# Kernel tuning notes

Measured on AMD Instinct MI355X. Metric: run time of the kernel, lower is better.

## Reference

```python
import jax, jax.numpy as jnp
import numpy as np

N_NODES = 50000
N_EDGES = 100000
IN_FEATS = 32
EDGE_FEATS = 32
HIDDEN = 32
OUT = 3


def setup_inputs() -> dict:
    key = jax.random.key(0)
    ks = jax.random.split(key, 16)
    s = 0.05
    return {
        "node_feats": jax.random.normal(ks[0], (N_NODES, IN_FEATS), jnp.float32),
        "edge_feats": jax.random.normal(ks[1], (N_EDGES, EDGE_FEATS), jnp.float32),
        "src": jax.random.randint(ks[2], (N_EDGES,), 0, N_NODES, jnp.int32),
        "dst": jax.random.randint(ks[3], (N_EDGES,), 0, N_NODES, jnp.int32),
        "edge_indices": jnp.arange(N_EDGES, dtype=jnp.int32),
        # edge_network: Linear(edge_feats, hidden*in) -> ReLU -> Linear(hidden*in, hidden*in)
        "W1": jax.random.normal(ks[4], (EDGE_FEATS, HIDDEN * IN_FEATS), jnp.float32) * s,
        "b1": jax.random.normal(ks[5], (HIDDEN * IN_FEATS,), jnp.float32) * s,
        "W2": jax.random.normal(ks[6], (HIDDEN * IN_FEATS, HIDDEN * IN_FEATS), jnp.float32) * s,
        "b2": jax.random.normal(ks[7], (HIDDEN * IN_FEATS,), jnp.float32) * s,
        # NNConv bias
        "conv_bias": jax.random.normal(ks[8], (HIDDEN,), jnp.float32) * s,
        # edge classifier: Linear(2*hidden+edge_feats, hidden) -> ReLU -> Linear(hidden, out)
        "Wc1": jax.random.normal(ks[9], (2 * HIDDEN + EDGE_FEATS, HIDDEN), jnp.float32) * s,
        "bc1": jax.random.normal(ks[10], (HIDDEN,), jnp.float32) * s,
        "Wc2": jax.random.normal(ks[11], (HIDDEN, OUT), jnp.float32) * s,
        "bc2": jax.random.normal(ks[12], (OUT,), jnp.float32) * s,
    }


def reference(node_feats, edge_feats, src, dst, edge_indices,
              W1, b1, W2, b2, conv_bias, Wc1, bc1, Wc2, bc2):
    N = node_feats.shape[0]
    E = edge_feats.shape[0]
    in_f = node_feats.shape[1]
    hid = conv_bias.shape[0]

    # edge-conditioned weights: MLP(efeat) -> [E, in, hidden]
    w = jax.nn.relu(edge_feats @ W1 + b1) @ W2 + b2
    w = w.reshape(E, in_f, hid)

    # per-edge matmul of gathered src features, then mean-aggregate into dst (DGL NNConv, aggregator='mean')
    msg = jnp.einsum("ei,eio->eo", node_feats[src], w)  # [E, hidden]
    agg = jax.ops.segment_sum(msg, dst, num_segments=N)  # [N, hidden]
    deg = jax.ops.segment_sum(jnp.ones((E,), msg.dtype), dst, num_segments=N)
    agg = agg / jnp.maximum(deg, 1.0)[:, None]
    h = jax.nn.relu(agg + conv_bias)  # [N, hidden]

    # gather-concat-MLP edge classifier
    s = src[edge_indices]
    d = dst[edge_indices]
    edge_in = jnp.concatenate([h[s], h[d], edge_feats[edge_indices]], axis=1)
    logits = jax.nn.relu(edge_in @ Wc1 + bc1) @ Wc2 + bc2
    return logits
```

## Files before the change

kernel.cpp:

```cpp
#include <hip/hip_runtime.h>
#include <hip/hip_bf16.h>
#include <stdint.h>

#define NNODES 50000
#define NEDGES 100000

typedef __attribute__((ext_vector_type(8))) short short8;
typedef __attribute__((ext_vector_type(4))) float f32x4;

__device__ __forceinline__ unsigned short f2bf(float f) {
    union { unsigned int i; float f; } v; v.f = f;
    unsigned int r = v.i + 0x7FFFu + ((v.i >> 16) & 1u);
    return (unsigned short)(r >> 16);
}
__device__ __forceinline__ float bf2f(unsigned short u) {
    union { unsigned int i; float f; } v; v.i = ((unsigned int)u) << 16; return v.f;
}
__device__ __forceinline__ void gload16(const void* g, void* lds) {
    __builtin_amdgcn_global_load_lds(
        (const __attribute__((address_space(1))) unsigned int*)g,
        (__attribute__((address_space(3))) unsigned int*)lds, 16, 0, 0);
}

__global__ __launch_bounds__(256) void k_pack(const float* __restrict__ W2,
                                              unsigned short* __restrict__ w2p) {
    const int idx = blockIdx.x * 256 + threadIdx.x;
    const int k = idx >> 10, col = idx & 1023;
    const float v = W2[idx];
    const int nb = col >> 7, n = col & 127;
    const int ks = k >> 5, kg = (k >> 3) & 3, j = k & 7;
    w2p[((((size_t)nb * 32 + ks) * 4 + kg) * 128 + n) * 8 + j] = f2bf(v);
}

__global__ __launch_bounds__(256) void k_packw1(const float* __restrict__ W1,
                                                unsigned short* __restrict__ w1pT) {
    const int idx = blockIdx.x * 256 + threadIdx.x;
    const int i = idx >> 10, col = idx & 1023;
    const float v = W1[idx];
    const int ks = col >> 5, c = col & 31;
    const int kt = c >> 4, lr = c & 15;
    const int lq = i >> 3, ii = i & 7;
    w1pT[((((size_t)ks * 2 + kt) * 4 + lq) * 16 + lr) * 8 + ii] = f2bf(v);
}

__global__ __launch_bounds__(256, 2) void k_gemm(
    const unsigned short* __restrict__ w2p, const unsigned short* __restrict__ w1pT,
    const float* __restrict__ ef, const float* __restrict__ nf,
    const float* __restrict__ b1, const float* __restrict__ b2,
    const int* __restrict__ src, const int* __restrict__ dst,
    float* __restrict__ agg, float* __restrict__ deg)
{
    __shared__ __align__(16) unsigned short sB[2][8192];
    __shared__ __align__(16) unsigned short sH[2][4096];
    __shared__ __align__(16) unsigned short sXb[4096];
    __shared__ int sD[128];

    const int t    = threadIdx.x;
    const int lane = t & 63;
    const int w    = t >> 6;
    const int wm   = w >> 1, wc = w & 1;
    const int lq   = lane >> 4, lr = lane & 15;
    const int e0   = blockIdx.x * 128;
    const int yb   = blockIdx.y;
    const int nblk0 = yb * 2;

    unsigned short* sE = sB[0];

    {
        const int e = t >> 1, fo = (t & 1) * 16;
        const int eg = e0 + e;
        const bool valid = eg < NEDGES;
        const int iq = fo >> 3;
        unsigned short hh[16];
        uint4 pa, pb;

        #pragma unroll
        for (int q = 0; q < 4; ++q) {
            float4 v = valid ? *(const float4*)(ef + (size_t)eg * 32 + fo + q * 4)
                             : float4{0.f, 0.f, 0.f, 0.f};
            hh[q*4+0] = f2bf(v.x); hh[q*4+1] = f2bf(v.y);
            hh[q*4+2] = f2bf(v.z); hh[q*4+3] = f2bf(v.w);
        }
        pa.x = hh[0] | ((unsigned)hh[1] << 16);  pa.y = hh[2]  | ((unsigned)hh[3] << 16);
        pa.z = hh[4] | ((unsigned)hh[5] << 16);  pa.w = hh[6]  | ((unsigned)hh[7] << 16);
        pb.x = hh[8] | ((unsigned)hh[9] << 16);  pb.y = hh[10] | ((unsigned)hh[11] << 16);
        pb.z = hh[12]| ((unsigned)hh[13] << 16); pb.w = hh[14] | ((unsigned)hh[15] << 16);
        *(uint4*)(sE + ((iq    ) * 128 + e) * 8) = pa;
        *(uint4*)(sE + ((iq + 1) * 128 + e) * 8) = pb;

        const int s = valid ? src[eg] : 0;
        #pragma unroll
        for (int q = 0; q < 4; ++q) {
            float4 xv = valid ? *(const float4*)(nf + (size_t)s * 32 + fo + q * 4)
                              : float4{0.f, 0.f, 0.f, 0.f};
            hh[q*4+0] = f2bf(xv.x); hh[q*4+1] = f2bf(xv.y);
            hh[q*4+2] = f2bf(xv.z); hh[q*4+3] = f2bf(xv.w);
        }
        pa.x = hh[0] | ((unsigned)hh[1] << 16);  pa.y = hh[2]  | ((unsigned)hh[3] << 16);
        pa.z = hh[4] | ((unsigned)hh[5] << 16);  pa.w = hh[6]  | ((unsigned)hh[7] << 16);
        pb.x = hh[8] | ((unsigned)hh[9] << 16);  pb.y = hh[10] | ((unsigned)hh[11] << 16);
        pb.z = hh[12]| ((unsigned)hh[13] << 16); pb.w = hh[14] | ((unsigned)hh[15] << 16);
        *(uint4*)(sXb + ((iq    ) * 128 + e) * 8) = pa;
        *(uint4*)(sXb + ((iq + 1) * 128 + e) * 8) = pb;
    }
    if (t < 128) {
        const int eg = e0 + t;
        const int dv = (eg < NEDGES) ? dst[eg] : -1;
        sD[t] = dv;
        if (yb == 0 && dv >= 0) atomicAdd(&deg[dv], 1.0f);
    }
    __syncthreads();

    const short8 bfe0 = *(const short8*)(sE + (lq * 128 + w * 32 + lr) * 8);
    const short8 bfe1 = *(const short8*)(sE + (lq * 128 + w * 32 + 16 + lr) * 8);

    f32x4 pm[8];
    #pragma unroll
    for (int i = 0; i < 8; ++i) pm[i] = f32x4{0.f, 0.f, 0.f, 0.f};
    if (yb == 0 && wc == 0) {
        short8 bb0, bb1;
        #pragma unroll
        for (int j = 0; j < 8; ++j) {
            bb0[j] = (short)f2bf(b2[(lq * 8 + j) * 32 + lr]);
            bb1[j] = (short)f2bf(b2[(lq * 8 + j) * 32 + 16 + lr]);
        }
        #pragma unroll
        for (int mt = 0; mt < 4; ++mt) {
            const short8 xf = *(const short8*)(sXb + (lq * 128 + wm * 64 + mt * 16 + lr) * 8);
            pm[mt * 2]     = __builtin_amdgcn_mfma_f32_16x16x32_bf16(xf, bb0, pm[mt * 2],     0, 0, 0);
            pm[mt * 2 + 1] = __builtin_amdgcn_mfma_f32_16x16x32_bf16(xf, bb1, pm[mt * 2 + 1], 0, 0, 0);
        }
    }
    __syncthreads();

    #define STAGE2(dstb, nblk_, ks_) do {                                          \
        const unsigned short* _g0 = w2p + ((size_t)((nblk_) * 32 + (ks_)) * 4096); \
        const unsigned short* _g1 = _g0 + (size_t)32 * 4096;                       \
        gload16(_g0 + (size_t)t * 8,         (dstb) + w * 512);                    \
        gload16(_g0 + (size_t)(t + 256) * 8, (dstb) + 2048 + w * 512);             \
        gload16(_g1 + (size_t)t * 8,         (dstb) + 4096 + w * 512);             \
        gload16(_g1 + (size_t)(t + 256) * 8, (dstb) + 6144 + w * 512);             \
    } while (0)

    STAGE2(sB[0], nblk0, 0);

    short8 w1c0 = *(const short8*)(w1pT + ((0 * 4 + lq) * 16 + lr) * 8);
    short8 w1c1 = *(const short8*)(w1pT + ((1 * 4 + lq) * 16 + lr) * 8);
    float4 b1c0 = *(const float4*)(b1 + lq * 4);
    float4 b1c1 = *(const float4*)(b1 + 16 + lq * 4);

    f32x4 acc[4][8];
    #pragma unroll
    for (int mt = 0; mt < 4; ++mt)
        #pragma unroll
        for (int nt = 0; nt < 8; ++nt) acc[mt][nt] = f32x4{0.f, 0.f, 0.f, 0.f};

    int buf = 0;
    for (int ks = 0; ks < 32; ++ks) {
        unsigned short* sHp = sH[ks & 1];

        f32x4 h00 = {b1c0.x, b1c0.y, b1c0.z, b1c0.w};
        f32x4 h01 = h00;
        f32x4 h10 = {b1c1.x, b1c1.y, b1c1.z, b1c1.w};
        f32x4 h11 = h10;
        h00 = __builtin_amdgcn_mfma_f32_16x16x32_bf16(w1c0, bfe0, h00, 0, 0, 0);
        h01 = __builtin_amdgcn_mfma_f32_16x16x32_bf16(w1c0, bfe1, h01, 0, 0, 0);
        h10 = __builtin_amdgcn_mfma_f32_16x16x32_bf16(w1c1, bfe0, h10, 0, 0, 0);
        h11 = __builtin_amdgcn_mfma_f32_16x16x32_bf16(w1c1, bfe1, h11, 0, 0, 0);

        #define STORE_H1(hv, kt, et) do {                                           \
            float r0 = fmaxf((hv)[0], 0.f), r1 = fmaxf((hv)[1], 0.f);               \
            float r2 = fmaxf((hv)[2], 0.f), r3 = fmaxf((hv)[3], 0.f);               \
            unsigned p0, p1;                                                         \
            asm("v_cvt_pk_bf16_f32 %0, %1, %2" : "=v"(p0) : "v"(r0), "v"(r1));       \
            asm("v_cvt_pk_bf16_f32 %0, %1, %2" : "=v"(p1) : "v"(r2), "v"(r3));       \
            uint2 pk; pk.x = p0; pk.y = p1;                                          \
            *(uint2*)(sHp + ((((kt) * 2 + (lq >> 1)) * 128 + w * 32 + (et) * 16 + lr)\
                * 8 + (lq & 1) * 4)) = pk;                                           \
        } while (0)
        STORE_H1(h00, 0, 0); STORE_H1(h01, 0, 1);
        STORE_H1(h10, 1, 0); STORE_H1(h11, 1, 1);
        #undef STORE_H1

        __syncthreads();

        if (ks != 31) STAGE2(sB[buf ^ 1], nblk0, ks + 1);
        const int nks2 = (ks == 31) ? 0 : ks + 1;
        short8 w1n0 = *(const short8*)(w1pT + ((((size_t)nks2 * 2 + 0) * 4 + lq) * 16 + lr) * 8);
        short8 w1n1 = *(const short8*)(w1pT + ((((size_t)nks2 * 2 + 1) * 4 + lq) * 16 + lr) * 8);
        float4 b1n0 = *(const float4*)(b1 + nks2 * 32 + lq * 4);
        float4 b1n1 = *(const float4*)(b1 + nks2 * 32 + 16 + lq * 4);

        const short8 af0 = *(const short8*)(sHp + (lq * 128 + wm * 64 +  0 + lr) * 8);
        const short8 af1 = *(const short8*)(sHp + (lq * 128 + wm * 64 + 16 + lr) * 8);
        const short8 af2 = *(const short8*)(sHp + (lq * 128 + wm * 64 + 32 + lr) * 8);
        const short8 af3 = *(const short8*)(sHp + (lq * 128 + wm * 64 + 48 + lr) * 8);
        const unsigned short* pb = sB[buf] + wc * 4096;
        __builtin_amdgcn_s_setprio(1);
        #pragma unroll
        for (int nt = 0; nt < 8; ++nt) {
            const short8 bf = *(const short8*)(pb + (lq * 128 + nt * 16 + lr) * 8);
            acc[0][nt] = __builtin_amdgcn_mfma_f32_16x16x32_bf16(af0, bf, acc[0][nt], 0, 0, 0);
            acc[1][nt] = __builtin_amdgcn_mfma_f32_16x16x32_bf16(af1, bf, acc[1][nt], 0, 0, 0);
            acc[2][nt] = __builtin_amdgcn_mfma_f32_16x16x32_bf16(af2, bf, acc[2][nt], 0, 0, 0);
            acc[3][nt] = __builtin_amdgcn_mfma_f32_16x16x32_bf16(af3, bf, acc[3][nt], 0, 0, 0);
        }
        __builtin_amdgcn_s_setprio(0);
        buf ^= 1;
        w1c0 = w1n0; w1c1 = w1n1; b1c0 = b1n0; b1c1 = b1n1;
    }

    {
        const int nblk = nblk0 + wc;
        #pragma unroll
        for (int ii = 0; ii < 4; ++ii) {
            const int i  = nblk * 4 + ii;
            const int iq = i >> 3, io = i & 7;
            #pragma unroll
            for (int mt = 0; mt < 4; ++mt)
                #pragma unroll
                for (int r = 0; r < 4; ++r) {
                    const int e = wm * 64 + mt * 16 + lq * 4 + r;
                    const float x = bf2f(sXb[iq * 1024 + e * 8 + io]);
                    pm[mt*2+0][r] = fmaf(x, acc[mt][ii*2+0][r], pm[mt*2+0][r]);
                    pm[mt*2+1][r] = fmaf(x, acc[mt][ii*2+1][r], pm[mt*2+1][r]);
                }
        }
    }
    #undef STAGE2

    __syncthreads();
    float* sRed = (float*)sB;
    if (wc == 0) {
        #pragma unroll
        for (int mt = 0; mt < 4; ++mt)
            #pragma unroll
            for (int r = 0; r < 4; ++r) {
                const int e = wm * 64 + mt * 16 + lq * 4 + r;
                sRed[e * 36 + lr]      = pm[mt*2][r];
                sRed[e * 36 + 16 + lr] = pm[mt*2+1][r];
            }
    }
    __syncthreads();
    if (wc == 1) {
        #pragma unroll
        for (int mt = 0; mt < 4; ++mt)
            #pragma unroll
            for (int r = 0; r < 4; ++r) {
                const int e = wm * 64 + mt * 16 + lq * 4 + r;
                sRed[e * 36 + lr]      += pm[mt*2][r];
                sRed[e * 36 + 16 + lr] += pm[mt*2+1][r];
            }
    }
    __syncthreads();

    #pragma unroll
    for (int mt = 0; mt < 2; ++mt)
        #pragma unroll
        for (int r = 0; r < 4; ++r) {
            const int e = w * 32 + mt * 16 + lq * 4 + r;
            const int d = sD[e];
            if (d >= 0) {
                atomicAdd(agg + (size_t)d * 32 + lr,      sRed[e * 36 + lr]);
                atomicAdd(agg + (size_t)d * 32 + 16 + lr, sRed[e * 36 + 16 + lr]);
            }
        }
}

__global__ __launch_bounds__(256) void k_node(
    float* __restrict__ agg, const float* __restrict__ deg,
    const float* __restrict__ cbias)
{
    const int idx = blockIdx.x * 256 + threadIdx.x;
    if (idx >= NNODES * 32) return;
    const int n = idx >> 5, o = idx & 31;
    const float d = fmaxf(deg[n], 1.0f);
    agg[idx] = fmaxf(agg[idx] / d + cbias[o], 0.0f);
}

__global__ __launch_bounds__(256) void k_cls(
    const float* __restrict__ h, const float* __restrict__ ef,
    const int* __restrict__ src, const int* __restrict__ dst,
    const int* __restrict__ eidx,
    const float* __restrict__ Wc1, const float* __restrict__ bc1,
    const float* __restrict__ Wc2, const float* __restrict__ bc2,
    float* __restrict__ out)
{
    __shared__ float s_w1[96 * 32];
    __shared__ float s_w2[96];
    __shared__ float s_b1[32];
    __shared__ float s_in[8][96];

    const int t = threadIdx.x;
    #pragma unroll
    for (int q = 0; q < 3; ++q)
        *(float4*)&s_w1[t * 12 + q * 4] = *(const float4*)&Wc1[t * 12 + q * 4];
    if (t < 96) s_w2[t] = Wc2[t];
    if (t >= 96 && t < 128) s_b1[t - 96] = bc1[t - 96];

    const int ee = t >> 5, l = t & 31;
    const int e  = blockIdx.x * 8 + ee;
    const int ei = eidx[e];
    const int s = src[ei], d = dst[ei];
    s_in[ee][l]      = h[(size_t)s * 32 + l];
    s_in[ee][32 + l] = h[(size_t)d * 32 + l];
    s_in[ee][64 + l] = ef[(size_t)ei * 32 + l];
    __syncthreads();

    float acc = s_b1[l];
    #pragma unroll
    for (int c = 0; c < 96; ++c) acc = fmaf(s_in[ee][c], s_w1[c * 32 + l], acc);
    acc = fmaxf(acc, 0.f);

    float p0 = acc * s_w2[l * 3 + 0];
    float p1 = acc * s_w2[l * 3 + 1];
    float p2 = acc * s_w2[l * 3 + 2];
    #pragma unroll
    for (int m = 1; m <= 16; m <<= 1) {
        p0 += __shfl_xor(p0, m);
        p1 += __shfl_xor(p1, m);
        p2 += __shfl_xor(p2, m);
    }
    if (l == 0) {
        out[(size_t)e * 3 + 0] = p0 + bc2[0];
        out[(size_t)e * 3 + 1] = p1 + bc2[1];
        out[(size_t)e * 3 + 2] = p2 + bc2[2];
    }
}

extern "C" void kernel_launch(void* const* d_in, const int* in_sizes, int n_in,
                              void* d_out, int out_size, void* d_ws, size_t ws_size,
                              hipStream_t stream) {
    const float* nf   = (const float*)d_in[0];
    const float* ef   = (const float*)d_in[1];
    const int*   src  = (const int*)d_in[2];
    const int*   dst  = (const int*)d_in[3];
    const int*   eidx = (const int*)d_in[4];
    const float* W1   = (const float*)d_in[5];
    const float* b1   = (const float*)d_in[6];
    const float* W2   = (const float*)d_in[7];
    const float* b2   = (const float*)d_in[8];
    const float* cb   = (const float*)d_in[9];
    const float* Wc1  = (const float*)d_in[10];
    const float* bc1  = (const float*)d_in[11];
    const float* Wc2  = (const float*)d_in[12];
    const float* bc2  = (const float*)d_in[13];
    float* out = (float*)d_out;

    float* agg = (float*)d_ws;
    float* deg = agg + (size_t)NNODES * 32;
    unsigned short* w2p  = (unsigned short*)(deg + NNODES);
    unsigned short* w1pT = w2p + 1048576;

    hipMemsetAsync(d_ws, 0, ((size_t)NNODES * 32 + NNODES) * 4, stream);
    k_pack<<<4096, 256, 0, stream>>>(W2, w2p);
    k_packw1<<<128, 256, 0, stream>>>(W1, w1pT);

    k_gemm<<<dim3((NEDGES + 127) / 128, 4), 256, 0, stream>>>(
        w2p, w1pT, ef, nf, b1, b2, src, dst, agg, deg);

    k_node<<<(NNODES * 32 + 255) / 256, 256, 0, stream>>>(agg, deg, cb);
    k_cls<<<NEDGES / 8, 256, 0, stream>>>(agg, ef, src, dst, eidx, Wc1, bc1, Wc2, bc2, out);
}
```

Before: 334.9 us.

## Switch edge-network GEMM to 32x32x16 MFMA and software-pipeline hidden-layer production

Replaces the 16x16x32 bf16 MFMA tiles with 32x32x16 tiles for the W1 hidden layer, the W2 GEMM, and the bias term, and repacks W1 to match the new operand layout. The next K-slice of the hidden activations is now produced while the current slice's B fragments are loaded, so each K step needs one barrier instead of two. The aim is fewer MFMA issues and LDS fragment reads per FLOP, plus less barrier stalling. The cost is more live registers (preloaded fragments for both k-chunks), which could hurt occupancy under launch_bounds(256,2).

```diff
diff --git a/kernel.cpp b/kernel.cpp
--- a/kernel.cpp
+++ b/kernel.cpp
@@ -7,6 +7,7 @@
 
 typedef __attribute__((ext_vector_type(8))) short short8;
 typedef __attribute__((ext_vector_type(4))) float f32x4;
+typedef __attribute__((ext_vector_type(16))) float f32x16;
 
 __device__ __forceinline__ unsigned short f2bf(float f) {
     union { unsigned int i; float f; } v; v.f = f;
@@ -35,12 +36,10 @@
 __global__ __launch_bounds__(256) void k_packw1(const float* __restrict__ W1,
                                                 unsigned short* __restrict__ w1pT) {
     const int idx = blockIdx.x * 256 + threadIdx.x;
-    const int i = idx >> 10, col = idx & 1023;
-    const float v = W1[idx];
-    const int ks = col >> 5, c = col & 31;
-    const int kt = c >> 4, lr = c & 15;
-    const int lq = i >> 3, ii = i & 7;
-    w1pT[((((size_t)ks * 2 + kt) * 4 + lq) * 16 + lr) * 8 + ii] = f2bf(v);
+    const int ii = idx & 7, lane = (idx >> 3) & 63, ic = (idx >> 9) & 1, ks = idx >> 10;
+    const int i = ic * 16 + (lane >> 5) * 8 + ii;
+    const int k = ks * 32 + (lane & 31);
+    w1pT[idx] = f2bf(W1[(size_t)i * 1024 + k]);
 }
 
 __global__ __launch_bounds__(256, 2) void k_gemm(
@@ -59,6 +58,7 @@
     const int lane = t & 63;
     const int w    = t >> 6;
     const int wm   = w >> 1, wc = w & 1;
+    const int lo5  = lane & 31, hi = lane >> 5;
     const int lq   = lane >> 4, lr = lane & 15;
     const int e0   = blockIdx.x * 128;
     const int yb   = blockIdx.y;
@@ -111,26 +111,63 @@
     }
     __syncthreads();
 
-    const short8 bfe0 = *(const short8*)(sE + (lq * 128 + w * 32 + lr) * 8);
-    const short8 bfe1 = *(const short8*)(sE + (lq * 128 + w * 32 + 16 + lr) * 8);
-
-    f32x4 pm[8];
-    #pragma unroll
-    for (int i = 0; i < 8; ++i) pm[i] = f32x4{0.f, 0.f, 0.f, 0.f};
+    const short8 bfe0 = *(const short8*)(sE + ((0 + hi) * 128 + w * 32 + lo5) * 8);
+    const short8 bfe1 = *(const short8*)(sE + ((2 + hi) * 128 + w * 32 + lo5) * 8);
+
+    f32x16 pm[2];
+    #pragma unroll
+    for (int mt = 0; mt < 2; ++mt)
+        #pragma unroll
+        for (int r = 0; r < 16; ++r) pm[mt][r] = 0.f;
     if (yb == 0 && wc == 0) {
-        short8 bb0, bb1;
-        #pragma unroll
-        for (int j = 0; j < 8; ++j) {
-            bb0[j] = (short)f2bf(b2[(lq * 8 + j) * 32 + lr]);
-            bb1[j] = (short)f2bf(b2[(lq * 8 + j) * 32 + 16 + lr]);
-        }
-        #pragma unroll
-        for (int mt = 0; mt < 4; ++mt) {
-            const short8 xf = *(const short8*)(sXb + (lq * 128 + wm * 64 + mt * 16 + lr) * 8);
-            pm[mt * 2]     = __builtin_amdgcn_mfma_f32_16x16x32_bf16(xf, bb0, pm[mt * 2],     0, 0, 0);
-            pm[mt * 2 + 1] = __builtin_amdgcn_mfma_f32_16x16x32_bf16(xf, bb1, pm[mt * 2 + 1], 0, 0, 0);
-        }
-    }
+        short8 b2f0, b2f1;
+        #pragma unroll
+        for (int ii = 0; ii < 8; ++ii) {
+            b2f0[ii] = (short)f2bf(b2[(     hi * 8 + ii) * 32 + lo5]);
+            b2f1[ii] = (short)f2bf(b2[(16 + hi * 8 + ii) * 32 + lo5]);
+        }
+        #pragma unroll
+        for (int mt = 0; mt < 2; ++mt) {
+            const short8 xa0 = *(const short8*)(sXb + ((0 + hi) * 128 + wm * 64 + mt * 32 + lo5) * 8);
+            const short8 xa1 = *(const short8*)(sXb + ((2 + hi) * 128 + wm * 64 + mt * 32 + lo5) * 8);
+            pm[mt] = __builtin_amdgcn_mfma_f32_32x32x16_bf16(xa0, b2f0, pm[mt], 0, 0, 0);
+            pm[mt] = __builtin_amdgcn_mfma_f32_32x32x16_bf16(xa1, b2f1, pm[mt], 0, 0, 0);
+        }
+    }
+
+    #define H1_PRODUCE(ks2_, dstp_, wA_, wB_) do {                                   \
+        f32x16 hacc;                                                                  \
+        _Pragma("unroll")                                                             \
+        for (int q = 0; q < 4; ++q) {                                                 \
+            const float4 blo = *(const float4*)(b1 + (ks2_) * 32 + q * 8);            \
+            const float4 bhi = *(const float4*)(b1 + (ks2_) * 32 + q * 8 + 4);        \
+            hacc[q*4+0] = hi ? bhi.x : blo.x;                                         \
+            hacc[q*4+1] = hi ? bhi.y : blo.y;                                         \
+            hacc[q*4+2] = hi ? bhi.z : blo.z;                                         \
+            hacc[q*4+3] = hi ? bhi.w : blo.w;                                         \
+        }                                                                             \
+        hacc = __builtin_amdgcn_mfma_f32_32x32x16_bf16((wA_), bfe0, hacc, 0, 0, 0);   \
+        hacc = __builtin_amdgcn_mfma_f32_32x32x16_bf16((wB_), bfe1, hacc, 0, 0, 0);   \
+        _Pragma("unroll")                                                             \
+        for (int q = 0; q < 4; ++q) {                                                 \
+            float v0 = fmaxf(hacc[q*4+0], 0.f), v1 = fmaxf(hacc[q*4+1], 0.f);         \
+            float v2 = fmaxf(hacc[q*4+2], 0.f), v3 = fmaxf(hacc[q*4+3], 0.f);         \
+            unsigned p0, p1;                                                          \
+            asm("v_cvt_pk_bf16_f32 %0, %1, %2" : "=v"(p0) : "v"(v0), "v"(v1));        \
+            asm("v_cvt_pk_bf16_f32 %0, %1, %2" : "=v"(p1) : "v"(v2), "v"(v3));        \
+            uint2 pk; pk.x = p0; pk.y = p1;                                           \
+            *(uint2*)((dstp_) + q * 1024 + (w * 32 + lo5) * 8 + hi * 4) = pk;         \
+        }                                                                             \
+    } while (0)
+
+    {
+        const short8 wA = *(const short8*)(w1pT + ((size_t)(0 * 2 + 0) * 64 + lane) * 8);
+        const short8 wB = *(const short8*)(w1pT + ((size_t)(0 * 2 + 1) * 64 + lane) * 8);
+        H1_PRODUCE(0, sH[0], wA, wB);
+    }
+    short8 w1cA = *(const short8*)(w1pT + ((size_t)(1 * 2 + 0) * 64 + lane) * 8);
+    short8 w1cB = *(const short8*)(w1pT + ((size_t)(1 * 2 + 1) * 64 + lane) * 8);
+
     __syncthreads();
 
     #define STAGE2(dstb, nblk_, ks_) do {                                          \
@@ -144,112 +181,87 @@
 
     STAGE2(sB[0], nblk0, 0);
 
-    short8 w1c0 = *(const short8*)(w1pT + ((0 * 4 + lq) * 16 + lr) * 8);
-    short8 w1c1 = *(const short8*)(w1pT + ((1 * 4 + lq) * 16 + lr) * 8);
-    float4 b1c0 = *(const float4*)(b1 + lq * 4);
-    float4 b1c1 = *(const float4*)(b1 + 16 + lq * 4);
-
-    f32x4 acc[4][8];
-    #pragma unroll
-    for (int mt = 0; mt < 4; ++mt)
-        #pragma unroll
-        for (int nt = 0; nt < 8; ++nt) acc[mt][nt] = f32x4{0.f, 0.f, 0.f, 0.f};
+    f32x16 acc[2][4];
+    #pragma unroll
+    for (int mt = 0; mt < 2; ++mt)
+        #pragma unroll
+        for (int nt = 0; nt < 4; ++nt)
+            #pragma unroll
+            for (int r = 0; r < 16; ++r) acc[mt][nt][r] = 0.f;
 
     int buf = 0;
     for (int ks = 0; ks < 32; ++ks) {
-        unsigned short* sHp = sH[ks & 1];
-
-        f32x4 h00 = {b1c0.x, b1c0.y, b1c0.z, b1c0.w};
-        f32x4 h01 = h00;
-        f32x4 h10 = {b1c1.x, b1c1.y, b1c1.z, b1c1.w};
-        f32x4 h11 = h10;
-        h00 = __builtin_amdgcn_mfma_f32_16x16x32_bf16(w1c0, bfe0, h00, 0, 0, 0);
-        h01 = __builtin_amdgcn_mfma_f32_16x16x32_bf16(w1c0, bfe1, h01, 0, 0, 0);
-        h10 = __builtin_amdgcn_mfma_f32_16x16x32_bf16(w1c1, bfe0, h10, 0, 0, 0);
-        h11 = __builtin_amdgcn_mfma_f32_16x16x32_bf16(w1c1, bfe1, h11, 0, 0, 0);
-
-        #define STORE_H1(hv, kt, et) do {                                           \
-            float r0 = fmaxf((hv)[0], 0.f), r1 = fmaxf((hv)[1], 0.f);               \
-            float r2 = fmaxf((hv)[2], 0.f), r3 = fmaxf((hv)[3], 0.f);               \
-            unsigned p0, p1;                                                         \
-            asm("v_cvt_pk_bf16_f32 %0, %1, %2" : "=v"(p0) : "v"(r0), "v"(r1));       \
-            asm("v_cvt_pk_bf16_f32 %0, %1, %2" : "=v"(p1) : "v"(r2), "v"(r3));       \
-            uint2 pk; pk.x = p0; pk.y = p1;                                          \
-            *(uint2*)(sHp + ((((kt) * 2 + (lq >> 1)) * 128 + w * 32 + (et) * 16 + lr)\
-                * 8 + (lq & 1) * 4)) = pk;                                           \
-        } while (0)
-        STORE_H1(h00, 0, 0); STORE_H1(h01, 0, 1);
-        STORE_H1(h10, 1, 0); STORE_H1(h11, 1, 1);
-        #undef STORE_H1
-
         __syncthreads();
 
         if (ks != 31) STAGE2(sB[buf ^ 1], nblk0, ks + 1);
-        const int nks2 = (ks == 31) ? 0 : ks + 1;
-        short8 w1n0 = *(const short8*)(w1pT + ((((size_t)nks2 * 2 + 0) * 4 + lq) * 16 + lr) * 8);
-        short8 w1n1 = *(const short8*)(w1pT + ((((size_t)nks2 * 2 + 1) * 4 + lq) * 16 + lr) * 8);
-        float4 b1n0 = *(const float4*)(b1 + nks2 * 32 + lq * 4);
-        float4 b1n1 = *(const float4*)(b1 + nks2 * 32 + 16 + lq * 4);
-
-        const short8 af0 = *(const short8*)(sHp + (lq * 128 + wm * 64 +  0 + lr) * 8);
-        const short8 af1 = *(const short8*)(sHp + (lq * 128 + wm * 64 + 16 + lr) * 8);
-        const short8 af2 = *(const short8*)(sHp + (lq * 128 + wm * 64 + 32 + lr) * 8);
-        const short8 af3 = *(const short8*)(sHp + (lq * 128 + wm * 64 + 48 + lr) * 8);
+
+        const unsigned short* pa = sH[ks & 1];
         const unsigned short* pb = sB[buf] + wc * 4096;
+        short8 af0[2], af1[2], bfr[2][4];
+        #pragma unroll
+        for (int kc = 0; kc < 2; ++kc) {
+            af0[kc] = *(const short8*)(pa + ((kc * 2 + hi) * 128 + wm * 64 +  0 + lo5) * 8);
+            af1[kc] = *(const short8*)(pa + ((kc * 2 + hi) * 128 + wm * 64 + 32 + lo5) * 8);
+            #pragma unroll
+            for (int nt = 0; nt < 4; ++nt)
+                bfr[kc][nt] = *(const short8*)(pb + ((kc * 2 + hi) * 128 + nt * 32 + lo5) * 8);
+        }
+
+        if (ks < 31) {
+            H1_PRODUCE(ks + 1, sH[(ks + 1) & 1], w1cA, w1cB);
+            const int nk2 = (ks < 30) ? ks + 2 : 31;
+            w1cA = *(const short8*)(w1pT + ((size_t)(nk2 * 2 + 0) * 64 + lane) * 8);
+            w1cB = *(const short8*)(w1pT + ((size_t)(nk2 * 2 + 1) * 64 + lane) * 8);
+        }
+
         __builtin_amdgcn_s_setprio(1);
         #pragma unroll
-        for (int nt = 0; nt < 8; ++nt) {
-            const short8 bf = *(const short8*)(pb + (lq * 128 + nt * 16 + lr) * 8);
-            acc[0][nt] = __builtin_amdgcn_mfma_f32_16x16x32_bf16(af0, bf, acc[0][nt], 0, 0, 0);
-            acc[1][nt] = __builtin_amdgcn_mfma_f32_16x16x32_bf16(af1, bf, acc[1][nt], 0, 0, 0);
-            acc[2][nt] = __builtin_amdgcn_mfma_f32_16x16x32_bf16(af2, bf, acc[2][nt], 0, 0, 0);
-            acc[3][nt] = __builtin_amdgcn_mfma_f32_16x16x32_bf16(af3, bf, acc[3][nt], 0, 0, 0);
+        for (int kc = 0; kc < 2; ++kc) {
+            #pragma unroll
+            for (int nt = 0; nt < 4; ++nt) {
+                acc[0][nt] = __builtin_amdgcn_mfma_f32_32x32x16_bf16(af0[kc], bfr[kc][nt], acc[0][nt], 0, 0, 0);
+                acc[1][nt] = __builtin_amdgcn_mfma_f32_32x32x16_bf16(af1[kc], bfr[kc][nt], acc[1][nt], 0, 0, 0);
+            }
         }
         __builtin_amdgcn_s_setprio(0);
         buf ^= 1;
-        w1c0 = w1n0; w1c1 = w1n1; b1c0 = b1n0; b1c1 = b1n1;
-    }
-
-    {
-        const int nblk = nblk0 + wc;
-        #pragma unroll
-        for (int ii = 0; ii < 4; ++ii) {
-            const int i  = nblk * 4 + ii;
-            const int iq = i >> 3, io = i & 7;
-            #pragma unroll
-            for (int mt = 0; mt < 4; ++mt)
-                #pragma unroll
-                for (int r = 0; r < 4; ++r) {
-                    const int e = wm * 64 + mt * 16 + lq * 4 + r;
-                    const float x = bf2f(sXb[iq * 1024 + e * 8 + io]);
-                    pm[mt*2+0][r] = fmaf(x, acc[mt][ii*2+0][r], pm[mt*2+0][r]);
-                    pm[mt*2+1][r] = fmaf(x, acc[mt][ii*2+1][r], pm[mt*2+1][r]);
-                }
-        }
     }
     #undef STAGE2
+    #undef H1_PRODUCE
+
+    #pragma unroll
+    for (int nt = 0; nt < 4; ++nt) {
+        const int i  = (nblk0 + wc) * 4 + nt;
+        const int iq = i >> 3, io = i & 7;
+        #pragma unroll
+        for (int mt = 0; mt < 2; ++mt)
+            #pragma unroll
+            for (int r = 0; r < 16; ++r) {
+                const int e = wm * 64 + mt * 32 + (r & 3) + 8 * (r >> 2) + 4 * hi;
+                const float x = bf2f(sXb[iq * 1024 + e * 8 + io]);
+                pm[mt][r] = fmaf(x, acc[mt][nt][r], pm[mt][r]);
+            }
+    }
 
     __syncthreads();
     float* sRed = (float*)sB;
     if (wc == 0) {
         #pragma unroll
-        for (int mt = 0; mt < 4; ++mt)
-            #pragma unroll
-            for (int r = 0; r < 4; ++r) {
-                const int e = wm * 64 + mt * 16 + lq * 4 + r;
-                sRed[e * 36 + lr]      = pm[mt*2][r];
-                sRed[e * 36 + 16 + lr] = pm[mt*2+1][r];
+        for (int mt = 0; mt < 2; ++mt)
+            #pragma unroll
+            for (int r = 0; r < 16; ++r) {
+                const int e = wm * 64 + mt * 32 + (r & 3) + 8 * (r >> 2) + 4 * hi;
+                sRed[e * 36 + lo5] = pm[mt][r];
             }
     }
     __syncthreads();
     if (wc == 1) {
         #pragma unroll
-        for (int mt = 0; mt < 4; ++mt)
-            #pragma unroll
-            for (int r = 0; r < 4; ++r) {
-                const int e = wm * 64 + mt * 16 + lq * 4 + r;
-                sRed[e * 36 + lr]      += pm[mt*2][r];
-                sRed[e * 36 + 16 + lr] += pm[mt*2+1][r];
+        for (int mt = 0; mt < 2; ++mt)
+            #pragma unroll
+            for (int r = 0; r < 16; ++r) {
+                const int e = wm * 64 + mt * 32 + (r & 3) + 8 * (r >> 2) + 4 * hi;
+                sRed[e * 36 + lo5] += pm[mt][r];
             }
     }
     __syncthreads();
```

Measured after the change: 356.8 us. 6.5% more time.
